# Performance work log

Hardware: AMD Instinct MI355X
Metric: run time of the kernel (lower is better)

## Reference

```python
import jax, jax.numpy as jnp
import numpy as np

STRIDE = 4
IMG_H, IMG_W = 800, 1216
NMS_THRESH = 0.7
PRE_NMS = 1000
POST_NMS = 1000
MIN_SIZE = 0.0
SCALE_CLAMP = float(np.log(1000.0 / 16.0))  # detectron2 Box2BoxTransform clamp
A = 3  # anchors per location


def _cell_anchors():
    size = 32.0
    ars = jnp.array([0.5, 1.0, 2.0], jnp.float32)
    area = size * size
    w = jnp.sqrt(area / ars)
    h = ars * w
    return jnp.stack([-w / 2, -h / 2, w / 2, h / 2], axis=1)  # [A,4]


def _anchors(H, W):
    sx = jnp.arange(W, dtype=jnp.float32) * STRIDE
    sy = jnp.arange(H, dtype=jnp.float32) * STRIDE
    gy, gx = jnp.meshgrid(sy, sx, indexing='ij')
    shifts = jnp.stack([gx, gy, gx, gy], axis=-1).reshape(-1, 1, 4)  # [H*W,1,4]
    return (shifts + _cell_anchors()[None]).reshape(-1, 4)  # [H*W*A,4]


def _conv(x, w, b, pad):
    y = jax.lax.conv_general_dilated(x, w, (1, 1), pad,
                                     dimension_numbers=('NCHW', 'OIHW', 'NCHW'))
    return y + b[None, :, None, None]


def _decode(anchors, deltas):
    # anchors [M,4], deltas [N,M,4]; weights (1,1,1,1)
    wa = anchors[:, 2] - anchors[:, 0]
    ha = anchors[:, 3] - anchors[:, 1]
    cx = anchors[:, 0] + 0.5 * wa
    cy = anchors[:, 1] + 0.5 * ha
    dx, dy = deltas[..., 0], deltas[..., 1]
    dw = jnp.minimum(deltas[..., 2], SCALE_CLAMP)
    dh = jnp.minimum(deltas[..., 3], SCALE_CLAMP)
    px = dx * wa + cx
    py = dy * ha + cy
    pw = jnp.exp(dw) * wa
    ph = jnp.exp(dh) * ha
    return jnp.stack([px - 0.5 * pw, py - 0.5 * ph,
                      px + 0.5 * pw, py + 0.5 * ph], axis=-1)


def _iou_matrix(boxes):  # [K,4] -> [K,K]
    area = (boxes[:, 2] - boxes[:, 0]) * (boxes[:, 3] - boxes[:, 1])
    lt = jnp.maximum(boxes[:, None, :2], boxes[None, :, :2])
    rb = jnp.minimum(boxes[:, None, 2:], boxes[None, :, 2:])
    wh = jnp.clip(rb - lt, 0.0)
    inter = wh[..., 0] * wh[..., 1]
    return inter / jnp.maximum(area[:, None] + area[None, :] - inter, 1e-9)


def _nms_keep(boxes):
    # boxes already sorted by descending score; greedy NMS
    iou = _iou_matrix(boxes)
    K = boxes.shape[0]

    def step(sup, i):
        keep = ~sup[i]
        sup = sup | (keep & (iou[i] > NMS_THRESH))
        return sup, keep

    _, keep = jax.lax.scan(step, jnp.zeros(K, bool), jnp.arange(K))
    return keep


def setup_inputs() -> dict:
    key = jax.random.key(0)
    ks = jax.random.split(key, 4)
    features = jax.random.normal(ks[0], (2, 256, 200, 304), jnp.float32)
    w_conv = jax.random.normal(ks[1], (256, 256, 3, 3), jnp.float32) * 0.01
    b_conv = jnp.zeros((256,), jnp.float32)
    w_obj = jax.random.normal(ks[2], (3, 256, 1, 1), jnp.float32) * 0.01
    b_obj = jnp.zeros((3,), jnp.float32)
    w_delta = jax.random.normal(ks[3], (12, 256, 1, 1), jnp.float32) * 0.01
    b_delta = jnp.zeros((12,), jnp.float32)
    return {"features": features, "w_conv": w_conv, "b_conv": b_conv,
            "w_obj": w_obj, "b_obj": b_obj, "w_delta": w_delta, "b_delta": b_delta}


def reference(features, w_conv, b_conv, w_obj, b_obj, w_delta, b_delta):
    N, C, H, W = features.shape
    t = jax.nn.relu(_conv(features, w_conv, b_conv, 'SAME'))
    logits = _conv(t, w_obj, b_obj, 'VALID')            # [N,A,H,W]
    deltas = _conv(t, w_delta, b_delta, 'VALID')        # [N,4A,H,W]
    logits = logits.transpose(0, 2, 3, 1).reshape(N, -1)               # [N,H*W*A]
    deltas = deltas.reshape(N, A, 4, H, W).transpose(0, 3, 4, 1, 2).reshape(N, -1, 4)

    anchors = _anchors(H, W)                             # [H*W*A,4]
    boxes = _decode(anchors, deltas)                     # [N,M,4]
    boxes = jnp.stack([jnp.clip(boxes[..., 0], 0.0, IMG_W),
                       jnp.clip(boxes[..., 1], 0.0, IMG_H),
                       jnp.clip(boxes[..., 2], 0.0, IMG_W),
                       jnp.clip(boxes[..., 3], 0.0, IMG_H)], axis=-1)

    valid = ((boxes[..., 2] - boxes[..., 0]) >= MIN_SIZE) & \
            ((boxes[..., 3] - boxes[..., 1]) >= MIN_SIZE)
    scores = jnp.where(valid, logits, -jnp.inf)

    top_s, top_i = jax.lax.top_k(scores, PRE_NMS)                      # sorted desc
    top_b = jnp.take_along_axis(boxes, top_i[..., None], axis=1)       # [N,K,4]

    keep = jax.vmap(_nms_keep)(top_b)                                  # [N,K]
    s = jnp.where(keep, top_s, -jnp.inf)
    fin_s, fin_i = jax.lax.top_k(s, POST_NMS)                          # sorted desc (=final sort)
    fin_b = jnp.take_along_axis(top_b, fin_i[..., None], axis=1)
    fin_b = jnp.where(jnp.isfinite(fin_s)[..., None], fin_b, 0.0)
    return fin_b, fin_s
```

## Files before the change

### kernel.cpp

```cpp
#include <hip/hip_runtime.h>
#include <math.h>
#include <stdint.h>

#define CC 256
#define HH 200
#define WW 304
#define NN 2
#define HW 60800
#define MM 182400
#define KK 1000
#define HP 202
#define WP 306
#define SCALE_CLAMP_F 4.135166556742356f
#define NEG_SENTINEL -1.0e30f
#define CAND_CAP 2048

typedef __attribute__((ext_vector_type(8))) short short8;
typedef __attribute__((ext_vector_type(4))) float f32x4;

__device__ __forceinline__ unsigned short f2bf(float f) {
  unsigned u = __float_as_uint(f);
  u += 0x7FFFu + ((u >> 16) & 1u);
  return (unsigned short)(u >> 16);
}
__device__ __forceinline__ unsigned int fkey(float s) {
  unsigned int u = __float_as_uint(s);
  return (u & 0x80000000u) ? ~u : (u | 0x80000000u);
}
__device__ __forceinline__ float iou_ref(float4 a, float4 b) {
#pragma clang fp contract(off)
  float areaA = (a.z - a.x) * (a.w - a.y);
  float areaB = (b.z - b.x) * (b.w - b.y);
  float ltx = fmaxf(a.x, b.x), lty = fmaxf(a.y, b.y);
  float rbx = fminf(a.z, b.z), rby = fminf(a.w, b.w);
  float w = fmaxf(rbx - ltx, 0.0f), h = fmaxf(rby - lty, 0.0f);
  float inter = w * h;
  float denom = fmaxf(areaA + areaB - inter, 1e-9f);
  return inter / denom;
}
__device__ __forceinline__ void gload16(const void* g, void* l) {
  __builtin_amdgcn_global_load_lds(
      (const __attribute__((address_space(1))) unsigned int*)g,
      (__attribute__((address_space(3))) unsigned int*)l, 16, 0, 0);
}
__device__ __forceinline__ int swz(int byte) {
  return byte ^ (((byte >> 7) & 7) << 4);
}

__global__ __launch_bounds__(256) void wt_pack(const float* __restrict__ w,
                                               unsigned short* __restrict__ wt_b) {
  int o = blockIdx.x * 256 + threadIdx.x;
  int cin = o & 255, cout = (o >> 8) & 255, pos = o >> 16;
  wt_b[o] = f2bf(w[(cout * 256 + cin) * 9 + pos]);
}

__global__ __launch_bounds__(256) void in_pack(const float* __restrict__ in,
                                               unsigned short* __restrict__ fbp) {
  __shared__ unsigned short tile[64][65];
  int tid = threadIdx.x;
  int p0 = blockIdx.x * 64;
  int c0 = blockIdx.y * 64;
  int n = blockIdx.z;
  int lane = tid & 63;
  int p = p0 + lane;
  int yp = 0, xp = 0;
  bool inb = false;
  if (p < HP * WP) {
    yp = p / WP; xp = p - yp * WP;
    inb = (yp >= 1 && yp <= HH && xp >= 1 && xp <= WW);
  }
  for (int ci = tid >> 6; ci < 64; ci += 4) {
    float v = 0.f;
    if (inb) v = in[(((size_t)n * CC + c0 + ci) * HH + (yp - 1)) * WW + (xp - 1)];
    tile[ci][lane] = f2bf(v);
  }
  __syncthreads();
  for (int i = 0; i < 4; ++i) {
    int idx4 = (i * 256 + tid) * 4;
    int hwi = idx4 >> 6, cb = idx4 & 63;
    int pp = p0 + hwi;
    if (pp < HP * WP) {
      ushort4 v;
      v.x = tile[cb][hwi]; v.y = tile[cb + 1][hwi];
      v.z = tile[cb + 2][hwi]; v.w = tile[cb + 3][hwi];
      *(ushort4*)&fbp[((size_t)n * HP * WP + pp) * 256 + c0 + cb] = v;
    }
  }
}

__global__ __launch_bounds__(256) void conv_mfma(
    const unsigned short* __restrict__ wt_b, const unsigned short* __restrict__ fbp,
    const float* __restrict__ bias, const float* __restrict__ w_obj,
    const float* __restrict__ w_delta, float* __restrict__ phead) {
  __shared__ __align__(16) unsigned short lA[2][4096];
  __shared__ __align__(16) unsigned short lB[2][5760];
  __shared__ float bl_l[128];
  int tid = threadIdx.x;
  int lane = tid & 63, wid = tid >> 6;
  int wm = wid >> 1, wn = wid & 1;
  int lrow = lane & 15, lgrp = lane >> 4;
  int zz = blockIdx.z;
  int n = zz >> 1, ct = zz & 1;
  int X0 = blockIdx.x * 16, Y0 = blockIdx.y * 8;

  f32x4 acc[4][4];
#pragma unroll
  for (int m = 0; m < 4; ++m)
#pragma unroll
    for (int r = 0; r < 4; ++r) acc[m][r] = {0.f, 0.f, 0.f, 0.f};

  if (tid < 128) bl_l[tid] = bias[ct * 128 + tid];

  auto stageA = [&](int pos, int cc, int buf) {
#pragma unroll
    for (int is = 0; is < 2; ++is) {
      int idx = is * 256 + tid;
      int L = swz(idx * 16);
      int cout = L >> 6, q = (L >> 4) & 3;
      const unsigned short* g =
          wt_b + (((size_t)pos * 256 + ct * 128 + cout) << 8) + cc * 32 + q * 8;
      gload16(g, (char*)&lA[buf][0] + is * 4096 + (wid << 10));
    }
  };
  auto stageB = [&](int cc, int buf) {
#pragma unroll
    for (int is = 0; is < 3; ++is) {
      int idx = is * 256 + tid;
      if (idx < 720) {
        int L = swz(idx * 16);
        int rc = L >> 6, q = (L >> 4) & 3;
        int row = rc / 18, col = rc - row * 18;
        const unsigned short* g =
            fbp + (((size_t)n * HP + Y0 + row) * WP + X0 + col) * 256 + cc * 32 + q * 8;
        gload16(g, (char*)&lB[buf][0] + is * 4096 + (wid << 10));
      }
    }
  };

  stageA(0, 0, 0);
  stageB(0, 0);
  __syncthreads();

  int ab = 0;
#pragma unroll 1
  for (int cc = 0; cc < 8; ++cc) {
    int bb = cc & 1;
#pragma unroll
    for (int pos = 0; pos < 9; ++pos) {
      if (pos < 8) stageA(pos + 1, cc, ab ^ 1);
      else if (cc < 7) stageA(0, cc + 1, ab ^ 1);
      if (pos == 0 && cc < 7) stageB(cc + 1, bb ^ 1);
      int ky = pos / 3, kx = pos - ky * 3;
      short8 af[4], bfr[4];
#pragma unroll
      for (int m = 0; m < 4; ++m) {
        int Lb = ((wm * 64 + m * 16 + lrow) << 6) + (lgrp << 4);
        af[m] = *(const short8*)((const char*)&lA[ab][0] + swz(Lb));
      }
#pragma unroll
      for (int r = 0; r < 4; ++r) {
        int Lb = (((wn * 4 + r + ky) * 18 + lrow + kx) << 6) + (lgrp << 4);
        bfr[r] = *(const short8*)((const char*)&lB[bb][0] + swz(Lb));
      }
#pragma unroll
      for (int m = 0; m < 4; ++m)
#pragma unroll
        for (int r = 0; r < 4; ++r)
          acc[m][r] = __builtin_amdgcn_mfma_f32_16x16x32_bf16(af[m], bfr[r], acc[m][r], 0, 0, 0);
      __syncthreads();
      ab ^= 1;
    }
  }

#pragma unroll
  for (int m = 0; m < 4; ++m)
#pragma unroll
    for (int j = 0; j < 4; ++j) {
      float b = bl_l[wm * 64 + m * 16 + (lgrp << 2) + j];
#pragma unroll
      for (int r = 0; r < 4; ++r) acc[m][r][j] = fmaxf(acc[m][r][j] + b, 0.f);
    }

  float* whl_l = (float*)&lA[0][0];
  for (int i = tid; i < 1920; i += 256) {
    int o = i >> 7, cl = i & 127;
    whl_l[i] = (o < 3) ? w_obj[o * 256 + ct * 128 + cl]
                       : w_delta[(o - 3) * 256 + ct * 128 + cl];
  }
  __syncthreads();

  float* hacc = (float*)&lB[0][0];
#pragma unroll 1
  for (int o = 0; o < 15; ++o) {
    float p0 = 0.f, p1 = 0.f, p2 = 0.f, p3 = 0.f;
#pragma unroll
    for (int m = 0; m < 4; ++m)
#pragma unroll
      for (int j = 0; j < 4; ++j) {
        float w = whl_l[o * 128 + wm * 64 + m * 16 + (lgrp << 2) + j];
        p0 = fmaf(w, acc[m][0][j], p0);
        p1 = fmaf(w, acc[m][1][j], p1);
        p2 = fmaf(w, acc[m][2][j], p2);
        p3 = fmaf(w, acc[m][3][j], p3);
      }
    p0 += __shfl_xor(p0, 16); p0 += __shfl_xor(p0, 32);
    p1 += __shfl_xor(p1, 16); p1 += __shfl_xor(p1, 32);
    p2 += __shfl_xor(p2, 16); p2 += __shfl_xor(p2, 32);
    p3 += __shfl_xor(p3, 16); p3 += __shfl_xor(p3, 32);
    if (lgrp == 0) {
      hacc[(((o * 8) + wn * 4 + 0) * 16 + lrow) * 2 + wm] = p0;
      hacc[(((o * 8) + wn * 4 + 1) * 16 + lrow) * 2 + wm] = p1;
      hacc[(((o * 8) + wn * 4 + 2) * 16 + lrow) * 2 + wm] = p2;
      hacc[(((o * 8) + wn * 4 + 3) * 16 + lrow) * 2 + wm] = p3;
    }
  }
  __syncthreads();

  if (tid < 128) {
    int row = tid >> 4, col = tid & 15;
    int loc = (Y0 + row) * WW + (X0 + col);
    size_t base = ((size_t)zz * 15) * HW + loc;
#pragma unroll
    for (int o = 0; o < 15; ++o) {
      const float* hp = &hacc[((o * 8 + row) * 16 + col) * 2];
      phead[base + (size_t)o * HW] = hp[0] + hp[1];
    }
  }
}

__global__ __launch_bounds__(256) void decode_kernel(
    const float* __restrict__ phead, const float* __restrict__ b_obj,
    const float* __restrict__ b_delta, float* __restrict__ scores,
    float* __restrict__ boxes, unsigned long long* __restrict__ keys) {
  int n = blockIdx.y;
  int loc = blockIdx.x * 256 + threadIdx.x;
  if (loc >= HW) return;
  float ho[15];
  const float* p0 = phead + ((size_t)(n * 2 + 0) * 15) * HW + loc;
  const float* p1 = phead + ((size_t)(n * 2 + 1) * 15) * HW + loc;
#pragma unroll
  for (int o = 0; o < 15; ++o) ho[o] = p0[(size_t)o * HW] + p1[(size_t)o * HW];
#pragma unroll
  for (int o = 0; o < 3; ++o) ho[o] += b_obj[o];
#pragma unroll
  for (int o = 0; o < 12; ++o) ho[3 + o] += b_delta[o];
  {
#pragma clang fp contract(off)
    int h = loc / WW, w = loc - h * WW;
    float gx = (float)(w * 4);
    float gy = (float)(h * 4);
    float s2048 = sqrtf(2048.0f), s512 = sqrtf(512.0f);
    float aw[3] = {s2048, 32.0f, s512};
    float ah[3] = {0.5f * s2048, 32.0f, 2.0f * s512};
#pragma unroll
    for (int a = 0; a < 3; ++a) {
      float ax1 = gx - 0.5f * aw[a], ay1 = gy - 0.5f * ah[a];
      float ax2 = gx + 0.5f * aw[a], ay2 = gy + 0.5f * ah[a];
      float wa = ax2 - ax1, ha = ay2 - ay1;
      float cx = ax1 + 0.5f * wa, cy = ay1 + 0.5f * ha;
      float dx = ho[3 + a * 4 + 0], dy = ho[3 + a * 4 + 1];
      float dw = fminf(ho[3 + a * 4 + 2], SCALE_CLAMP_F);
      float dh = fminf(ho[3 + a * 4 + 3], SCALE_CLAMP_F);
      float px = dx * wa + cx, py = dy * ha + cy;
      float pw = expf(dw) * wa, ph = expf(dh) * ha;
      float x1 = px - 0.5f * pw, y1 = py - 0.5f * ph;
      float x2v = px + 0.5f * pw, y2v = py + 0.5f * ph;
      x1 = fminf(fmaxf(x1, 0.f), 1216.f);
      y1 = fminf(fmaxf(y1, 0.f), 800.f);
      x2v = fminf(fmaxf(x2v, 0.f), 1216.f);
      y2v = fminf(fmaxf(y2v, 0.f), 800.f);
      int m = loc * 3 + a;
      ((float4*)boxes)[(size_t)n * MM + m] = make_float4(x1, y1, x2v, y2v);
      float sc = ho[a];
      scores[(size_t)n * MM + m] = sc;
      keys[(size_t)n * MM + m] =
          ((unsigned long long)fkey(sc) << 18) | (unsigned long long)(262143 - m);
    }
  }
}

__global__ __launch_bounds__(256) void zero_hist(unsigned int* __restrict__ ghist,
                                                 unsigned int* __restrict__ cnt) {
  int i = blockIdx.x * 256 + threadIdx.x;
  if (i < 2 * 8192) ghist[i] = 0;
  if (i < 2) cnt[i] = 0;
}

__global__ __launch_bounds__(256) void hist_kernel(const unsigned long long* __restrict__ keys,
                                                   unsigned int* __restrict__ ghist) {
  __shared__ unsigned int h[8192];
  int tid = threadIdx.x, n = blockIdx.y;
  for (int i = tid; i < 8192; i += 256) h[i] = 0;
  __syncthreads();
  const unsigned long long* kp = keys + (size_t)n * MM;
  int i0 = blockIdx.x * 2850, i1 = min(i0 + 2850, MM);
  for (int i = i0 + tid; i < i1; i += 256)
    atomicAdd(&h[(unsigned)(kp[i] >> 37)], 1u);
  __syncthreads();
  for (int i = tid; i < 8192; i += 256)
    if (h[i]) atomicAdd(&ghist[n * 8192 + i], h[i]);
}

__global__ __launch_bounds__(256) void pick_kernel(const unsigned int* __restrict__ ghist,
                                                   int* __restrict__ thrbin) {
  int n = blockIdx.x, tid = threadIdx.x;
  __shared__ unsigned int ps[256];
  const unsigned int* h = ghist + n * 8192;
  unsigned s = 0;
  for (int k = 0; k < 32; ++k) s += h[tid * 32 + k];
  ps[tid] = s;
  __syncthreads();
  if (tid == 0) {
    unsigned cum = 0; int b = 0;
    for (int t = 255; t >= 0; --t) {
      if (cum + ps[t] >= KK) {
        for (int bin = t * 32 + 31; bin >= t * 32; --bin) {
          cum += h[bin];
          if (cum >= KK) { b = bin; break; }
        }
        break;
      }
      cum += ps[t];
    }
    thrbin[n] = b;
  }
}

__global__ __launch_bounds__(256) void gather_kernel(
    const unsigned long long* __restrict__ keys, const int* __restrict__ thrbin,
    unsigned int* __restrict__ cnt, unsigned long long* __restrict__ cand) {
  int n = blockIdx.y;
  int b = thrbin[n];
  const unsigned long long* kp = keys + (size_t)n * MM;
  int i0 = blockIdx.x * 2850, i1 = min(i0 + 2850, MM);
  for (int i = i0 + threadIdx.x; i < i1; i += 256) {
    unsigned long long k = kp[i];
    if ((int)(unsigned)(k >> 37) >= b) {
      unsigned pos = atomicAdd(&cnt[n], 1u);
      if (pos < CAND_CAP) cand[(size_t)n * CAND_CAP + pos] = k;
    }
  }
}

__global__ __launch_bounds__(1024) void final_select(
    const unsigned long long* __restrict__ cand, const unsigned int* __restrict__ cnt,
    const float* __restrict__ scores, const float* __restrict__ boxes,
    float* __restrict__ s_scores, float* __restrict__ s_boxes) {
  __shared__ unsigned long long sel[CAND_CAP];
  int n = blockIdx.x, tid = threadIdx.x;
  int E = (int)min(cnt[n], (unsigned)CAND_CAP);
  for (int i = tid; i < CAND_CAP; i += 1024)
    sel[i] = (i < E) ? cand[(size_t)n * CAND_CAP + i] : 0ull;
  __syncthreads();
  for (unsigned k2 = 2; k2 <= CAND_CAP; k2 <<= 1) {
    for (unsigned j = k2 >> 1; j > 0; j >>= 1) {
      for (int i = tid; i < CAND_CAP; i += 1024) {
        int l = i ^ (int)j;
        if (l > i) {
          unsigned long long a = sel[i], bb = sel[l];
          bool sw = ((i & k2) == 0) ? (a < bb) : (a > bb);
          if (sw) { sel[i] = bb; sel[l] = a; }
        }
      }
      __syncthreads();
    }
  }
  if (tid < KK) {
    unsigned long long k = sel[tid];
    int m = 262143 - (int)(k & 0x3FFFFull);
    s_scores[n * KK + tid] = scores[(size_t)n * MM + m];
    ((float4*)s_boxes)[n * KK + tid] = ((const float4*)boxes)[(size_t)n * MM + m];
  }
}

__global__ __launch_bounds__(256) void mask_kernel(const float* __restrict__ s_boxes,
                                                   unsigned long long* __restrict__ mask) {
  int i = blockIdx.x, n = blockIdx.y;
  int tid = threadIdx.x, w = tid >> 6, lane = tid & 63;
  const float4* bp = (const float4*)s_boxes + n * KK;
  float4 bi = bp[i];
#pragma unroll
  for (int p = 0; p < 4; ++p) {
    int word = p * 4 + w;
    int j = word * 64 + lane;
    bool over = false;
    if (j < KK) {
      float4 bj = bp[j];
      over = iou_ref(bi, bj) > 0.7f;
    }
    unsigned long long bal = __ballot(over);
    if (lane == 0) mask[((size_t)n * KK + i) * 16 + word] = bal;
  }
}

__global__ __launch_bounds__(1024) void scan_write_kernel(
    const float* __restrict__ s_scores, const float* __restrict__ s_boxes,
    const unsigned long long* __restrict__ mask, float* __restrict__ out) {
  int n = blockIdx.x, tid = threadIdx.x;
  int wid = tid >> 6, lane = tid & 63;
  __shared__ unsigned long long swl[16];
  __shared__ unsigned long long keepw[16];
  __shared__ unsigned int wpre[17];
  if (tid < 16) swl[tid] = 0ull;
  __syncthreads();
  const unsigned long long* mrow = mask + (size_t)n * 16000;
  for (int c = 0; c < 16; ++c) {
    int i = c * 64 + lane;
    unsigned long long myword = (i < KK) ? mrow[(size_t)i * 16 + wid] : 0ull;
    if (wid == 0) {
      unsigned long long m = (i < KK) ? mrow[(size_t)i * 16 + c] : 0ull;
      unsigned long long cur = swl[c];
      unsigned long long kw = 0ull;
      int lim = min(64, KK - c * 64);
      for (int b = 0; b < lim; ++b) {
        unsigned long long mb = __shfl(m, b);
        if (!((cur >> b) & 1ull)) { kw |= (1ull << b); cur |= mb; }
      }
      if (lane == 0) keepw[c] = kw;
    }
    __syncthreads();
    unsigned long long kw = keepw[c];
    unsigned long long v = ((kw >> lane) & 1ull) ? myword : 0ull;
#pragma unroll
    for (int s = 32; s > 0; s >>= 1) v |= __shfl_xor(v, s);
    if (lane == 0) swl[wid] |= v;
    __syncthreads();
  }
  if (tid == 0) {
    unsigned int c = 0;
    for (int w2 = 0; w2 < 16; ++w2) { wpre[w2] = c; c += (unsigned int)__popcll(keepw[w2]); }
    wpre[16] = c;
  }
  __syncthreads();
  if (tid < KK) {
    int word = tid >> 6, bit = tid & 63;
    unsigned long long kwv = keepw[word];
    bool kept = (kwv >> bit) & 1ull;
    unsigned int before = wpre[word] + (unsigned int)__popcll(kwv & ((1ull << bit) - 1ull));
    unsigned int nk = wpre[16];
    unsigned int dst = kept ? before : nk + ((unsigned int)tid - before);
    float4 b = kept ? ((const float4*)s_boxes)[n * KK + tid] : make_float4(0.f, 0.f, 0.f, 0.f);
    float s = kept ? s_scores[n * KK + tid] : NEG_SENTINEL;
    ((float4*)out)[n * KK + dst] = b;
    out[8000 + n * KK + dst] = s;
  }
}

extern "C" void kernel_launch(void* const* d_in, const int* in_sizes, int n_in,
                              void* d_out, int out_size, void* d_ws, size_t ws_size,
                              hipStream_t stream) {
  (void)in_sizes; (void)n_in; (void)out_size; (void)ws_size;
  const float* features = (const float*)d_in[0];
  const float* w_conv   = (const float*)d_in[1];
  const float* b_conv   = (const float*)d_in[2];
  const float* w_obj    = (const float*)d_in[3];
  const float* b_obj    = (const float*)d_in[4];
  const float* w_delta  = (const float*)d_in[5];
  const float* b_delta  = (const float*)d_in[6];

  char* ws = (char*)d_ws;
  unsigned short* wt_b = (unsigned short*)ws;
  unsigned short* fbp  = (unsigned short*)(ws + 1179648);
  char* O = ws + 64475136;
  float* phead = (float*)O;
  float* scores = (float*)(O + 14592000);
  float* boxes  = (float*)(O + 16051200);
  unsigned long long* keys = (unsigned long long*)(O + 21888000);
  char* P = O + 24806400;
  unsigned int* ghist = (unsigned int*)P;
  int* thrbin = (int*)(P + 65536);
  unsigned int* cnt = (unsigned int*)(P + 65792);
  unsigned long long* cand = (unsigned long long*)(P + 66048);
  float* s_scores = (float*)(P + 98816);
  float* s_boxes  = (float*)(P + 107008);
  unsigned long long* maskbuf = (unsigned long long*)(P + 139264);
  float* out = (float*)d_out;

  wt_pack<<<2304, 256, 0, stream>>>(w_conv, wt_b);
  in_pack<<<dim3(966, 4, 2), 256, 0, stream>>>(features, fbp);
  conv_mfma<<<dim3(19, 25, 4), 256, 0, stream>>>(wt_b, fbp, b_conv, w_obj, w_delta, phead);
  decode_kernel<<<dim3(238, 2), 256, 0, stream>>>(phead, b_obj, b_delta,
                                                  scores, boxes, keys);
  zero_hist<<<64, 256, 0, stream>>>(ghist, cnt);
  hist_kernel<<<dim3(64, 2), 256, 0, stream>>>(keys, ghist);
  pick_kernel<<<2, 256, 0, stream>>>(ghist, thrbin);
  gather_kernel<<<dim3(64, 2), 256, 0, stream>>>(keys, thrbin, cnt, cand);
  final_select<<<2, 1024, 0, stream>>>(cand, cnt, scores, boxes, s_scores, s_boxes);
  mask_kernel<<<dim3(1000, 2), 256, 0, stream>>>(s_boxes, maskbuf);
  scan_write_kernel<<<2, 1024, 0, stream>>>(s_scores, s_boxes, maskbuf, out);
}
```

Before: 392.3 us.

## Triple-buffer conv weight tiles with vmcnt waits; fuse histogram into decode

```diff
diff --git a/kernel.cpp b/kernel.cpp
--- a/kernel.cpp
+++ b/kernel.cpp
@@ -17,6 +17,8 @@
 
 typedef __attribute__((ext_vector_type(8))) short short8;
 typedef __attribute__((ext_vector_type(4))) float f32x4;
+
+#define VMW(N) asm volatile("s_waitcnt vmcnt(" #N ")" ::: "memory")
 
 __device__ __forceinline__ unsigned short f2bf(float f) {
   unsigned u = __float_as_uint(f);
@@ -92,7 +94,7 @@
     const unsigned short* __restrict__ wt_b, const unsigned short* __restrict__ fbp,
     const float* __restrict__ bias, const float* __restrict__ w_obj,
     const float* __restrict__ w_delta, float* __restrict__ phead) {
-  __shared__ __align__(16) unsigned short lA[2][4096];
+  __shared__ __align__(16) unsigned short lA[3][4096];
   __shared__ __align__(16) unsigned short lB[2][5760];
   __shared__ float bl_l[128];
   int tid = threadIdx.x;
@@ -138,24 +140,29 @@
   };
 
   stageA(0, 0, 0);
+  stageA(1, 0, 1);
   stageB(0, 0);
   __syncthreads();
 
-  int ab = 0;
 #pragma unroll 1
   for (int cc = 0; cc < 8; ++cc) {
-    int bb = cc & 1;
+    const int bb = cc & 1;
+    const bool ccl7 = (cc < 7);
 #pragma unroll
     for (int pos = 0; pos < 9; ++pos) {
-      if (pos < 8) stageA(pos + 1, cc, ab ^ 1);
-      else if (cc < 7) stageA(0, cc + 1, ab ^ 1);
-      if (pos == 0 && cc < 7) stageB(cc + 1, bb ^ 1);
+      {
+        int pos2 = pos + 2, cc2 = cc;
+        if (pos2 >= 9) { pos2 -= 9; cc2 += 1; }
+        if (cc2 < 8) stageA(pos2, cc2, (pos + 2) % 3);
+      }
+      if (pos == 0 && ccl7) stageB(cc + 1, bb ^ 1);
+
       int ky = pos / 3, kx = pos - ky * 3;
       short8 af[4], bfr[4];
 #pragma unroll
       for (int m = 0; m < 4; ++m) {
         int Lb = ((wm * 64 + m * 16 + lrow) << 6) + (lgrp << 4);
-        af[m] = *(const short8*)((const char*)&lA[ab][0] + swz(Lb));
+        af[m] = *(const short8*)((const char*)&lA[pos % 3][0] + swz(Lb));
       }
 #pragma unroll
       for (int r = 0; r < 4; ++r) {
@@ -167,10 +174,20 @@
 #pragma unroll
         for (int r = 0; r < 4; ++r)
           acc[m][r] = __builtin_amdgcn_mfma_f32_16x16x32_bf16(af[m], bfr[r], acc[m][r], 0, 0, 0);
-      __syncthreads();
-      ab ^= 1;
-    }
-  }
+
+      if (pos < 2) {
+        if (ccl7) VMW(5); else VMW(2);
+      } else if (pos == 7) {
+        if (ccl7) VMW(2); else VMW(0);
+      } else {
+        VMW(2);
+      }
+      __builtin_amdgcn_sched_barrier(0);
+      __builtin_amdgcn_s_barrier();
+      asm volatile("" ::: "memory");
+    }
+  }
+  __syncthreads();
 
 #pragma unroll
   for (int m = 0; m < 4; ++m)
@@ -231,80 +248,73 @@
 __global__ __launch_bounds__(256) void decode_kernel(
     const float* __restrict__ phead, const float* __restrict__ b_obj,
     const float* __restrict__ b_delta, float* __restrict__ scores,
-    float* __restrict__ boxes, unsigned long long* __restrict__ keys) {
+    float* __restrict__ boxes, unsigned long long* __restrict__ keys,
+    unsigned int* __restrict__ ghist) {
+  __shared__ unsigned int hl[8192];
+  int tid = threadIdx.x;
+  for (int i = tid; i < 8192; i += 256) hl[i] = 0;
+  __syncthreads();
   int n = blockIdx.y;
-  int loc = blockIdx.x * 256 + threadIdx.x;
-  if (loc >= HW) return;
-  float ho[15];
-  const float* p0 = phead + ((size_t)(n * 2 + 0) * 15) * HW + loc;
-  const float* p1 = phead + ((size_t)(n * 2 + 1) * 15) * HW + loc;
-#pragma unroll
-  for (int o = 0; o < 15; ++o) ho[o] = p0[(size_t)o * HW] + p1[(size_t)o * HW];
-#pragma unroll
-  for (int o = 0; o < 3; ++o) ho[o] += b_obj[o];
-#pragma unroll
-  for (int o = 0; o < 12; ++o) ho[3 + o] += b_delta[o];
-  {
+  int loc = blockIdx.x * 256 + tid;
+  if (loc < HW) {
+    float ho[15];
+    const float* p0 = phead + ((size_t)(n * 2 + 0) * 15) * HW + loc;
+    const float* p1 = phead + ((size_t)(n * 2 + 1) * 15) * HW + loc;
+#pragma unroll
+    for (int o = 0; o < 15; ++o) ho[o] = p0[(size_t)o * HW] + p1[(size_t)o * HW];
+#pragma unroll
+    for (int o = 0; o < 3; ++o) ho[o] += b_obj[o];
+#pragma unroll
+    for (int o = 0; o < 12; ++o) ho[3 + o] += b_delta[o];
+    {
 #pragma clang fp contract(off)
-    int h = loc / WW, w = loc - h * WW;
-    float gx = (float)(w * 4);
-    float gy = (float)(h * 4);
-    float s2048 = sqrtf(2048.0f), s512 = sqrtf(512.0f);
-    float aw[3] = {s2048, 32.0f, s512};
-    float ah[3] = {0.5f * s2048, 32.0f, 2.0f * s512};
-#pragma unroll
-    for (int a = 0; a < 3; ++a) {
-      float ax1 = gx - 0.5f * aw[a], ay1 = gy - 0.5f * ah[a];
-      float ax2 = gx + 0.5f * aw[a], ay2 = gy + 0.5f * ah[a];
-      float wa = ax2 - ax1, ha = ay2 - ay1;
-      float cx = ax1 + 0.5f * wa, cy = ay1 + 0.5f * ha;
-      float dx = ho[3 + a * 4 + 0], dy = ho[3 + a * 4 + 1];
-      float dw = fminf(ho[3 + a * 4 + 2], SCALE_CLAMP_F);
-      float dh = fminf(ho[3 + a * 4 + 3], SCALE_CLAMP_F);
-      float px = dx * wa + cx, py = dy * ha + cy;
-      float pw = expf(dw) * wa, ph = expf(dh) * ha;
-      float x1 = px - 0.5f * pw, y1 = py - 0.5f * ph;
-      float x2v = px + 0.5f * pw, y2v = py + 0.5f * ph;
-      x1 = fminf(fmaxf(x1, 0.f), 1216.f);
-      y1 = fminf(fmaxf(y1, 0.f), 800.f);
-      x2v = fminf(fmaxf(x2v, 0.f), 1216.f);
-      y2v = fminf(fmaxf(y2v, 0.f), 800.f);
-      int m = loc * 3 + a;
-      ((float4*)boxes)[(size_t)n * MM + m] = make_float4(x1, y1, x2v, y2v);
-      float sc = ho[a];
-      scores[(size_t)n * MM + m] = sc;
-      keys[(size_t)n * MM + m] =
-          ((unsigned long long)fkey(sc) << 18) | (unsigned long long)(262143 - m);
-    }
-  }
-}
-
-__global__ __launch_bounds__(256) void zero_hist(unsigned int* __restrict__ ghist,
-                                                 unsigned int* __restrict__ cnt) {
-  int i = blockIdx.x * 256 + threadIdx.x;
-  if (i < 2 * 8192) ghist[i] = 0;
-  if (i < 2) cnt[i] = 0;
-}
-
-__global__ __launch_bounds__(256) void hist_kernel(const unsigned long long* __restrict__ keys,
-                                                   unsigned int* __restrict__ ghist) {
-  __shared__ unsigned int h[8192];
-  int tid = threadIdx.x, n = blockIdx.y;
-  for (int i = tid; i < 8192; i += 256) h[i] = 0;
-  __syncthreads();
-  const unsigned long long* kp = keys + (size_t)n * MM;
-  int i0 = blockIdx.x * 2850, i1 = min(i0 + 2850, MM);
-  for (int i = i0 + tid; i < i1; i += 256)
-    atomicAdd(&h[(unsigned)(kp[i] >> 37)], 1u);
-  __syncthreads();
-  for (int i = tid; i < 8192; i += 256)
-    if (h[i]) atomicAdd(&ghist[n * 8192 + i], h[i]);
-}
-
-__global__ __launch_bounds__(256) void pick_kernel(const unsigned int* __restrict__ ghist,
-                                                   int* __restrict__ thrbin) {
-  int n = blockIdx.x, tid = threadIdx.x;
+      int h = loc / WW, w = loc - h * WW;
+      float gx = (float)(w * 4);
+      float gy = (float)(h * 4);
+      float s2048 = sqrtf(2048.0f), s512 = sqrtf(512.0f);
+      float aw[3] = {s2048, 32.0f, s512};
+      float ah[3] = {0.5f * s2048, 32.0f, 2.0f * s512};
+#pragma unroll
+      for (int a = 0; a < 3; ++a) {
+        float ax1 = gx - 0.5f * aw[a], ay1 = gy - 0.5f * ah[a];
+        float ax2 = gx + 0.5f * aw[a], ay2 = gy + 0.5f * ah[a];
+        float wa = ax2 - ax1, ha = ay2 - ay1;
+        float cx = ax1 + 0.5f * wa, cy = ay1 + 0.5f * ha;
+        float dx = ho[3 + a * 4 + 0], dy = ho[3 + a * 4 + 1];
+        float dw = fminf(ho[3 + a * 4 + 2], SCALE_CLAMP_F);
+        float dh = fminf(ho[3 + a * 4 + 3], SCALE_CLAMP_F);
+        float px = dx * wa + cx, py = dy * ha + cy;
+        float pw = expf(dw) * wa, ph = expf(dh) * ha;
+        float x1 = px - 0.5f * pw, y1 = py - 0.5f * ph;
+        float x2v = px + 0.5f * pw, y2v = py + 0.5f * ph;
+        x1 = fminf(fmaxf(x1, 0.f), 1216.f);
+        y1 = fminf(fmaxf(y1, 0.f), 800.f);
+        x2v = fminf(fmaxf(x2v, 0.f), 1216.f);
+        y2v = fminf(fmaxf(y2v, 0.f), 800.f);
+        int m = loc * 3 + a;
+        ((float4*)boxes)[(size_t)n * MM + m] = make_float4(x1, y1, x2v, y2v);
+        float sc = ho[a];
+        scores[(size_t)n * MM + m] = sc;
+        unsigned long long k =
+            ((unsigned long long)fkey(sc) << 18) | (unsigned long long)(262143 - m);
+        keys[(size_t)n * MM + m] = k;
+        atomicAdd(&hl[(unsigned)(k >> 37)], 1u);
+      }
+    }
+  }
+  __syncthreads();
+  for (int i = tid; i < 8192; i += 256) {
+    unsigned v = hl[i];
+    if (v) atomicAdd(&ghist[n * 8192 + i], v);
+  }
+}
+
+__global__ __launch_bounds__(256) void gather_kernel(
+    const unsigned long long* __restrict__ keys, const unsigned int* __restrict__ ghist,
+    unsigned int* __restrict__ cnt, unsigned long long* __restrict__ cand) {
   __shared__ unsigned int ps[256];
+  __shared__ int bsh;
+  int n = blockIdx.y, tid = threadIdx.x;
   const unsigned int* h = ghist + n * 8192;
   unsigned s = 0;
   for (int k = 0; k < 32; ++k) s += h[tid * 32 + k];
@@ -322,18 +332,13 @@
       }
       cum += ps[t];
     }
-    thrbin[n] = b;
-  }
-}
-
-__global__ __launch_bounds__(256) void gather_kernel(
-    const unsigned long long* __restrict__ keys, const int* __restrict__ thrbin,
-    unsigned int* __restrict__ cnt, unsigned long long* __restrict__ cand) {
-  int n = blockIdx.y;
-  int b = thrbin[n];
+    bsh = b;
+  }
+  __syncthreads();
+  int b = bsh;
   const unsigned long long* kp = keys + (size_t)n * MM;
   int i0 = blockIdx.x * 2850, i1 = min(i0 + 2850, MM);
-  for (int i = i0 + threadIdx.x; i < i1; i += 256) {
+  for (int i = i0 + tid; i < i1; i += 256) {
     unsigned long long k = kp[i];
     if ((int)(unsigned)(k >> 37) >= b) {
       unsigned pos = atomicAdd(&cnt[n], 1u);
@@ -468,23 +473,20 @@
   unsigned long long* keys = (unsigned long long*)(O + 21888000);
   char* P = O + 24806400;
   unsigned int* ghist = (unsigned int*)P;
-  int* thrbin = (int*)(P + 65536);
-  unsigned int* cnt = (unsigned int*)(P + 65792);
-  unsigned long long* cand = (unsigned long long*)(P + 66048);
-  float* s_scores = (float*)(P + 98816);
-  float* s_boxes  = (float*)(P + 107008);
+  unsigned int* cnt = (unsigned int*)(P + 65536);
+  unsigned long long* cand = (unsigned long long*)(P + 65792);
+  float* s_scores = (float*)(P + 98560);
+  float* s_boxes  = (float*)(P + 106752);
   unsigned long long* maskbuf = (unsigned long long*)(P + 139264);
   float* out = (float*)d_out;
 
   wt_pack<<<2304, 256, 0, stream>>>(w_conv, wt_b);
   in_pack<<<dim3(966, 4, 2), 256, 0, stream>>>(features, fbp);
+  hipMemsetAsync(ghist, 0, 65536 + 256, stream);
   conv_mfma<<<dim3(19, 25, 4), 256, 0, stream>>>(wt_b, fbp, b_conv, w_obj, w_delta, phead);
   decode_kernel<<<dim3(238, 2), 256, 0, stream>>>(phead, b_obj, b_delta,
-                                                  scores, boxes, keys);
-  zero_hist<<<64, 256, 0, stream>>>(ghist, cnt);
-  hist_kernel<<<dim3(64, 2), 256, 0, stream>>>(keys, ghist);
-  pick_kernel<<<2, 256, 0, stream>>>(ghist, thrbin);
-  gather_kernel<<<dim3(64, 2), 256, 0, stream>>>(keys, thrbin, cnt, cand);
+                                                  scores, boxes, keys, ghist);
+  gather_kernel<<<dim3(64, 2), 256, 0, stream>>>(keys, ghist, cnt, cand);
   final_select<<<2, 1024, 0, stream>>>(cand, cnt, scores, boxes, s_scores, s_boxes);
   mask_kernel<<<dim3(1000, 2), 256, 0, stream>>>(s_boxes, maskbuf);
   scan_write_kernel<<<2, 1024, 0, stream>>>(s_scores, s_boxes, maskbuf, out);
```

Measured after the change: 395.6 us. No clear change (+0.8%).
